# Kernel optimization log

Measured on AMD Instinct MI355X. Metric: run time of the kernel, lower is better.

## Reference

```python
import jax, jax.numpy as jnp
import numpy as np
import math

H = 256; W = 256
NUM_CURVES = 256
NUM_SAMPLES = 32
NUM_BEZIERS = 2
BDEG = 5            # Bernstein degree used by the module (bezier_degree+1)
CTRL_STRIDE = 5     # bezier_degree+1; segments share endpoints, wrap (closed curve)
N_CTRL = NUM_BEZIERS * CTRL_STRIDE   # 10 control points per closed curve
PIX_CHUNK = 512
CHOLESKY_BOUND = jnp.array([0.5, 0.0, 0.5], jnp.float32)


def _bernstein():
    # t in linspace(0.007, 0.993, S) exactly as _update_bernstein_cache
    t = jnp.linspace(0.007, 0.993, NUM_SAMPLES)
    i = jnp.arange(BDEG + 1, dtype=jnp.float32)
    comb = jnp.array([math.comb(BDEG, k) for k in range(BDEG + 1)], jnp.float32)
    return comb * (t[:, None] ** i) * ((1.0 - t[:, None]) ** (BDEG - i))  # [S, BDEG+1]


def _render(control_points, features_dc, cholesky, opacity, depth, background):
    Bmat = _bernstein()
    # closed curve: segment k uses control points (k*5 + j) mod 10, j=0..5
    seg_idx = (jnp.arange(NUM_BEZIERS)[:, None] * CTRL_STRIDE
               + jnp.arange(BDEG + 1)[None, :]) % N_CTRL          # [K, 6]
    seg_ctrl = control_points[:, seg_idx]                          # [N, K, 6, 2]
    pts = jnp.einsum('sj,nkjd->nksd', Bmat, seg_ctrl)              # [N, K, S, 2]
    pts = pts.reshape(NUM_CURVES, -1, 2)                           # [N, Gper, 2]
    gper = pts.shape[1]

    # normalized [-1,1] -> pixel coords
    means = (jnp.tanh(pts) * 0.5 + 0.5) * jnp.array([W, H], jnp.float32)
    means = means.reshape(-1, 2)                                   # [G, 2]

    # 2x2 covariance from lower-triangular Cholesky (per curve)
    c = cholesky + CHOLESKY_BOUND[None, :]                         # l11, l21, l22
    s00 = c[:, 0] ** 2
    s01 = c[:, 0] * c[:, 1]
    s11 = c[:, 1] ** 2 + c[:, 2] ** 2
    det = s00 * s11 - s01 ** 2
    conic = jnp.stack([s11 / det, -s01 / det, s00 / det], -1)      # [N, 3]

    rep = lambda a: jnp.repeat(a, gper, axis=0)
    conic_g = rep(conic)                                           # [G, 3]
    color_g = rep(jax.nn.sigmoid(features_dc))                     # [G, 3]
    alpha_g = rep(jax.nn.sigmoid(opacity))[:, 0]                   # [G]
    depth_g = rep(depth)[:, 0]                                     # [G]

    order = jnp.argsort(depth_g)                                   # front-to-back
    means_s = means[order]
    conic_s = conic_g[order]
    color_s = color_g[order]
    alpha_s = alpha_g[order]

    ys, xs = jnp.meshgrid(jnp.arange(H, dtype=jnp.float32) + 0.5,
                          jnp.arange(W, dtype=jnp.float32) + 0.5, indexing='ij')
    pix = jnp.stack([xs.ravel(), ys.ravel()], -1).reshape(-1, PIX_CHUNK, 2)

    @jax.checkpoint
    def render_chunk(p):                                           # [C,2] -> [C,3]
        dx = p[:, None, 0] - means_s[None, :, 0]
        dy = p[:, None, 1] - means_s[None, :, 1]
        power = (-0.5 * (conic_s[None, :, 0] * dx * dx
                         + conic_s[None, :, 2] * dy * dy)
                 - conic_s[None, :, 1] * dx * dy)
        a = jnp.clip(alpha_s[None, :] * jnp.exp(power), 0.0, 0.999)
        logT = jnp.cumsum(jnp.log1p(-a), axis=1)
        t_excl = jnp.exp(logT - jnp.log1p(-a))   # transmittance before each splat
        rgb = (a * t_excl) @ color_s             # [C, 3]
        return rgb + jnp.exp(logT[:, -1:]) * background[None, :]

    img = jax.lax.map(render_chunk, pix)                           # [P/C, C, 3]
    return jnp.clip(img.reshape(H, W, 3), 0.0, 1.0)


def setup_inputs() -> dict:
    key = jax.random.key(0)
    k1, k2, k3, k4 = jax.random.split(key, 4)
    return {
        "control_points": jax.random.normal(k1, (NUM_CURVES, N_CTRL, 2), jnp.float32),
        "features_dc": jax.random.uniform(k2, (NUM_CURVES, 3), jnp.float32),
        "cholesky": jax.random.uniform(k3, (NUM_CURVES, 3), jnp.float32),
        "opacity": jnp.ones((NUM_CURVES, 1), jnp.float32),
        "depth": jax.random.uniform(k4, (NUM_CURVES, 1), jnp.float32),
        "background": jnp.ones((3,), jnp.float32),
    }


def reference(control_points, features_dc, cholesky, opacity, depth, background):
    return _render(control_points, features_dc, cholesky, opacity, depth, background)
```

## Files before the change

kernel.cpp:

```cpp
#include <hip/hip_runtime.h>
#include <math.h>

#define NCURVES   256
#define GPER      64
#define NUM_G     (NCURVES*GPER)
#define IMG_W     256
#define IMG_H     256
#define TILE      16
#define TILES_X   (IMG_W/TILE)
#define TILES_Y   (IMG_H/TILE)
#define NTILES    (TILES_X*TILES_Y)
#define REC_F     12
#define SEGS      16
#define GSEG      (NUM_G/SEGS)
#define NSUB      (GSEG/256)

#define A_MIN     3.0e-6f
#define P_CUT     (-12.6f)
#define T_EPS     1.0e-5f

__global__ __launch_bounds__(GPER)
void prep(const float* __restrict__ ctrl,
          const float* __restrict__ features,
          const float* __restrict__ cholesky,
          const float* __restrict__ opacity,
          const float* __restrict__ depth,
          float*       __restrict__ recs,
          unsigned*    __restrict__ bbox)
{
    int c   = blockIdx.x;
    int tid = threadIdx.x;

    float dc = depth[c];
    int r = 0;
    #pragma unroll
    for (int jj = 0; jj < 4; ++jj) {
        int j = tid + jj*64;
        float dj = depth[j];
        r += (dj < dc) || (dj == dc && j < c);
    }
    #pragma unroll
    for (int off = 32; off > 0; off >>= 1) r += __shfl_down(r, off, 64);
    r = __shfl(r, 0, 64);

    float c0 = cholesky[3*c+0] + 0.5f;
    float c1 = cholesky[3*c+1];
    float c2 = cholesky[3*c+2] + 0.5f;
    float s00 = c0*c0;
    float s01 = c0*c1;
    float s11 = c1*c1 + c2*c2;
    float inv = 1.0f / (s00*s11 - s01*s01);
    float A  =  s11*inv;
    float Bc = -s01*inv;
    float Cc =  s00*inv;

    float cr = 1.0f/(1.0f + __expf(-features[3*c+0]));
    float cg = 1.0f/(1.0f + __expf(-features[3*c+1]));
    float cb = 1.0f/(1.0f + __expf(-features[3*c+2]));
    float al = 1.0f/(1.0f + __expf(-opacity[c]));

    float cut = fmaxf(2.0f*(__logf(al) - __logf(A_MIN)), 0.0f);
    float rx = sqrtf(cut * s00);
    float ry = sqrtf(cut * s11);

    int k = tid >> 5;
    int s = tid & 31;
    float t = 0.007f + (float)s * (0.986f/31.0f);
    float u = 1.0f - t;
    float t2=t*t, t3=t2*t, t4=t3*t, t5=t4*t;
    float u2=u*u, u3=u2*u, u4=u3*u, u5=u4*u;
    float w[6] = { u5, 5.0f*t*u4, 10.0f*t2*u3, 10.0f*t3*u2, 5.0f*t4*u, t5 };

    const float* cp = ctrl + c*20;
    float px = 0.0f, py = 0.0f;
    #pragma unroll
    for (int j = 0; j < 6; ++j) {
        int idx = (k*5 + j) % 10;
        px += w[j]*cp[2*idx+0];
        py += w[j]*cp[2*idx+1];
    }
    float mx = (tanhf(px)*0.5f + 0.5f) * (float)IMG_W;
    float my = (tanhf(py)*0.5f + 0.5f) * (float)IMG_H;

    int gi = r*GPER + tid;
    float* o = recs + (size_t)gi*REC_F;
    o[0]=mx; o[1]=my; o[2]=A; o[3]=Bc; o[4]=Cc; o[5]=al;
    o[6]=cr; o[7]=cg; o[8]=cb; o[9]=0.0f; o[10]=0.0f; o[11]=0.0f;

    int tx0 = min(max((int)floorf((mx - rx) * (1.0f/TILE)), 0), TILES_X-1);
    int tx1 = min(max((int)floorf((mx + rx) * (1.0f/TILE)), 0), TILES_X-1);
    int ty0 = min(max((int)floorf((my - ry) * (1.0f/TILE)), 0), TILES_Y-1);
    int ty1 = min(max((int)floorf((my + ry) * (1.0f/TILE)), 0), TILES_Y-1);
    bbox[gi] = (unsigned)tx0 | ((unsigned)ty0<<8) | ((unsigned)tx1<<16) | ((unsigned)ty1<<24);
}

__global__ __launch_bounds__(256)
void render_seg(const float*    __restrict__ recs,
                const unsigned* __restrict__ bbox,
                float4*         __restrict__ partial)
{
    __shared__ float4   data[256][3];
    __shared__ unsigned wcnt[4];

    int tid   = threadIdx.x;
    int seg   = blockIdx.x & (SEGS-1);
    int tile  = blockIdx.x >> 4;
    int tilex = tile & (TILES_X-1);
    int tiley = tile >> 4;
    int X = tilex*TILE + (tid & (TILE-1));
    int Y = tiley*TILE + (tid >> 4);
    float px = (float)X + 0.5f;
    float py = (float)Y + 0.5f;

    int lane = tid & 63;
    int wid  = tid >> 6;
    unsigned long long lmask = (1ull << lane) - 1ull;

    int gbeg = seg * GSEG;

    bool pred[NSUB];
    {
        unsigned bb[NSUB];
        #pragma unroll
        for (int b = 0; b < NSUB; ++b) bb[b] = bbox[gbeg + b*256 + tid];
        #pragma unroll
        for (int b = 0; b < NSUB; ++b) {
            unsigned v = bb[b];
            int tx0 =  v        & 0xff;
            int ty0 = (v >> 8)  & 0xff;
            int tx1 = (v >> 16) & 0xff;
            int ty1 = (v >> 24) & 0xff;
            pred[b] = (tilex >= tx0) & (tilex <= tx1) & (tiley >= ty0) & (tiley <= ty1);
        }
    }

    float T = 1.0f, accr = 0.0f, accg = 0.0f, accb = 0.0f;

    #pragma unroll 1
    for (int b = 0; b < NSUB; ++b) {
        unsigned long long m = __ballot(pred[b] ? 1 : 0);
        if (lane == 0) wcnt[wid] = (unsigned)__popcll(m);

        int nalive = __syncthreads_count(T > T_EPS);
        if (nalive == 0) break;

        unsigned c0 = wcnt[0], c1 = wcnt[1], c2 = wcnt[2], c3 = wcnt[3];
        int total = (int)(c0 + c1 + c2 + c3);
        if (total) {
            if (pred[b]) {
                unsigned woff = (wid > 0 ? c0 : 0u) + (wid > 1 ? c1 : 0u) + (wid > 2 ? c2 : 0u);
                int slot = (int)(woff + (unsigned)__popcll(m & lmask));
                const float4* rp = (const float4*)(recs + (size_t)(gbeg + b*256 + tid)*REC_F);
                float4 d0 = rp[0], d1 = rp[1], d2 = rp[2];
                data[slot][0] = d0;
                data[slot][1] = d1;
                data[slot][2] = d2;
            }
            __syncthreads();

            if (T > T_EPS) {
                for (int j = 0; j < total; ++j) {
                    float4 q0 = data[j][0];
                    float4 q1 = data[j][1];
                    float  cb_ = data[j][2].x;
                    float dx = px - q0.x;
                    float dy = py - q0.y;
                    float p  = -0.5f*(q0.z*dx*dx + q1.x*dy*dy) - q0.w*dx*dy;
                    if (p > P_CUT) {
                        float a = q1.y * __expf(p);
                        a = fminf(a, 0.999f);
                        float wgt = a * T;
                        accr += wgt * q1.z;
                        accg += wgt * q1.w;
                        accb += wgt * cb_;
                        T *= (1.0f - a);
                        if (T < T_EPS) break;
                    }
                }
            }
        }
    }

    partial[(size_t)seg*(IMG_W*IMG_H) + (size_t)Y*IMG_W + X] =
        make_float4(accr, accg, accb, T);
}

__global__ __launch_bounds__(256)
void combine(const float4* __restrict__ partial,
             const float*  __restrict__ background,
             float*        __restrict__ out)
{
    int p = blockIdx.x * 256 + threadIdx.x;

    float accr = 0.0f, accg = 0.0f, accb = 0.0f, T = 1.0f;
    #pragma unroll
    for (int s = 0; s < SEGS; ++s) {
        float4 q = partial[(size_t)s*(IMG_W*IMG_H) + p];
        accr += T * q.x;
        accg += T * q.y;
        accb += T * q.z;
        T    *= q.w;
    }
    float r = fminf(fmaxf(accr + T*background[0], 0.0f), 1.0f);
    float g = fminf(fmaxf(accg + T*background[1], 0.0f), 1.0f);
    float b = fminf(fmaxf(accb + T*background[2], 0.0f), 1.0f);

    size_t oi = (size_t)p*3;
    out[oi+0] = r;
    out[oi+1] = g;
    out[oi+2] = b;
}

extern "C" void kernel_launch(void* const* d_in, const int* in_sizes, int n_in,
                              void* d_out, int out_size, void* d_ws, size_t ws_size,
                              hipStream_t stream)
{
    const float* ctrl       = (const float*)d_in[0];
    const float* features   = (const float*)d_in[1];
    const float* cholesky   = (const float*)d_in[2];
    const float* opacity    = (const float*)d_in[3];
    const float* depth      = (const float*)d_in[4];
    const float* background = (const float*)d_in[5];
    float* out = (float*)d_out;

    char* w = (char*)d_ws;
    float*    recs    = (float*)   (w);
    unsigned* bboxp   = (unsigned*)(w + 786432);
    float4*   partial = (float4*)  (w + 786432 + 65536);

    prep<<<NCURVES, GPER, 0, stream>>>(ctrl, features, cholesky, opacity, depth,
                                       recs, bboxp);
    render_seg<<<SEGS*NTILES, 256, 0, stream>>>(recs, bboxp, partial);
    combine<<<(IMG_W*IMG_H)/256, 256, 0, stream>>>(partial, background, out);
}
```

Baseline: 93.42 us.

## Precompute ballot counts and double-buffer shared splat data to halve barriers

Computes all sub-batch ballots and per-wave counts up front with a single barrier. The main loop then skips empty batches and double-buffers the shared splat records, so each batch needs only one barrier instead of two. This cuts synchronisation cost per batch. In exchange it uses twice the shared memory, which may reduce occupancy.

New measurement: 93.69 us. No clear change (+0.3%).

```diff
diff --git a/kernel.cpp b/kernel.cpp
--- a/kernel.cpp
+++ b/kernel.cpp
@@ -99,8 +99,8 @@
                 const unsigned* __restrict__ bbox,
                 float4*         __restrict__ partial)
 {
-    __shared__ float4   data[256][3];
-    __shared__ unsigned wcnt[4];
+    __shared__ float4   data[2][256][3];
+    __shared__ unsigned wcnt[NSUB][4];
 
     int tid   = threadIdx.x;
     int seg   = blockIdx.x & (SEGS-1);
@@ -134,48 +134,61 @@
         }
     }
 
+    unsigned long long m[NSUB];
+    #pragma unroll
+    for (int b = 0; b < NSUB; ++b) {
+        m[b] = __ballot(pred[b] ? 1 : 0);
+        if (lane == 0) wcnt[b][wid] = (unsigned)__popcll(m[b]);
+    }
+    __syncthreads();
+
+    int      total[NSUB];
+    unsigned woff[NSUB];
+    #pragma unroll
+    for (int b = 0; b < NSUB; ++b) {
+        unsigned c0 = wcnt[b][0], c1 = wcnt[b][1], c2 = wcnt[b][2], c3 = wcnt[b][3];
+        total[b] = (int)(c0 + c1 + c2 + c3);
+        woff[b]  = (wid > 0 ? c0 : 0u) + (wid > 1 ? c1 : 0u) + (wid > 2 ? c2 : 0u);
+    }
+
     float T = 1.0f, accr = 0.0f, accg = 0.0f, accb = 0.0f;
+    int nb = 0;
 
     #pragma unroll 1
     for (int b = 0; b < NSUB; ++b) {
-        unsigned long long m = __ballot(pred[b] ? 1 : 0);
-        if (lane == 0) wcnt[wid] = (unsigned)__popcll(m);
-
+        if (total[b] == 0) continue;
+        int buf = nb & 1;
+        ++nb;
+
+        if (pred[b]) {
+            int slot = (int)(woff[b] + (unsigned)__popcll(m[b] & lmask));
+            const float4* rp = (const float4*)(recs + (size_t)(gbeg + b*256 + tid)*REC_F);
+            float4 d0 = rp[0], d1 = rp[1], d2 = rp[2];
+            data[buf][slot][0] = d0;
+            data[buf][slot][1] = d1;
+            data[buf][slot][2] = d2;
+        }
         int nalive = __syncthreads_count(T > T_EPS);
         if (nalive == 0) break;
 
-        unsigned c0 = wcnt[0], c1 = wcnt[1], c2 = wcnt[2], c3 = wcnt[3];
-        int total = (int)(c0 + c1 + c2 + c3);
-        if (total) {
-            if (pred[b]) {
-                unsigned woff = (wid > 0 ? c0 : 0u) + (wid > 1 ? c1 : 0u) + (wid > 2 ? c2 : 0u);
-                int slot = (int)(woff + (unsigned)__popcll(m & lmask));
-                const float4* rp = (const float4*)(recs + (size_t)(gbeg + b*256 + tid)*REC_F);
-                float4 d0 = rp[0], d1 = rp[1], d2 = rp[2];
-                data[slot][0] = d0;
-                data[slot][1] = d1;
-                data[slot][2] = d2;
-            }
-            __syncthreads();
-
-            if (T > T_EPS) {
-                for (int j = 0; j < total; ++j) {
-                    float4 q0 = data[j][0];
-                    float4 q1 = data[j][1];
-                    float  cb_ = data[j][2].x;
-                    float dx = px - q0.x;
-                    float dy = py - q0.y;
-                    float p  = -0.5f*(q0.z*dx*dx + q1.x*dy*dy) - q0.w*dx*dy;
-                    if (p > P_CUT) {
-                        float a = q1.y * __expf(p);
-                        a = fminf(a, 0.999f);
-                        float wgt = a * T;
-                        accr += wgt * q1.z;
-                        accg += wgt * q1.w;
-                        accb += wgt * cb_;
-                        T *= (1.0f - a);
-                        if (T < T_EPS) break;
-                    }
+        if (T > T_EPS) {
+            int tot = total[b];
+            for (int j = 0; j < tot; ++j) {
+                float4 q0 = data[buf][j][0];
+                float4 q1 = data[buf][j][1];
+                float  cb_ = data[buf][j][2].x;
+                float dx = px - q0.x;
+                float dy = py - q0.y;
+                float p  = -0.5f*(q0.z*dx*dx + q1.x*dy*dy) - q0.w*dx*dy;
+                if (p > P_CUT) {
+                    float a = q1.y * __expf(p);
+                    a = fminf(a, 0.999f);
+                    float wgt = a * T;
+                    accr += wgt * q1.z;
+                    accg += wgt * q1.w;
+                    accb += wgt * cb_;
+                    T *= (1.0f - a);
+                    if (T < T_EPS) break;
                 }
             }
         }
```
